# Kernel tuning notes

Hardware: AMD Instinct MI355X
Metric: run time of the kernel (lower is better)

## Reference

```python
import jax, jax.numpy as jnp
import numpy as np

B_, L_, D_MODEL = 2, 2048, 1024
D_INNER, D_STATE, DT_RANK, D_CONV = 2048, 16, 64, 4


def setup_inputs() -> dict:
    key = jax.random.key(0)
    ks = jax.random.split(key, 8)
    x = jax.random.normal(ks[0], (B_, L_, D_MODEL), dtype=jnp.float32)
    W_in = jax.random.normal(ks[1], (D_MODEL, 2 * D_INNER), dtype=jnp.float32) / np.sqrt(D_MODEL)
    conv_w = jax.random.normal(ks[2], (D_INNER, 1, D_CONV), dtype=jnp.float32) / np.sqrt(D_CONV)
    conv_b = jnp.zeros((D_INNER,), dtype=jnp.float32)
    W_x = jax.random.normal(ks[3], (D_INNER, DT_RANK + 2 * D_STATE), dtype=jnp.float32) / np.sqrt(D_INNER)
    W_dt = jax.random.normal(ks[4], (DT_RANK, D_INNER), dtype=jnp.float32) / np.sqrt(DT_RANK)
    b_dt = jax.random.normal(ks[5], (D_INNER,), dtype=jnp.float32) * 0.01
    A_log = jnp.log(jnp.broadcast_to(jnp.arange(1, D_STATE + 1, dtype=jnp.float32), (D_INNER, D_STATE)))
    D = jnp.ones((D_INNER,), dtype=jnp.float32)
    W_out = jax.random.normal(ks[6], (D_INNER, D_MODEL), dtype=jnp.float32) / np.sqrt(D_INNER)
    return {"x": x, "W_in": W_in, "conv_w": conv_w, "conv_b": conv_b, "W_x": W_x,
            "W_dt": W_dt, "b_dt": b_dt, "A_log": A_log, "D": D, "W_out": W_out}


def _mamba_fwd(x, W_in, conv_w, conv_b, W_x, W_dt, b_dt, A_log, D, W_out):
    b, l, d = x.shape
    x_and_res = x @ W_in                      # [b, l, 2*d_inner]
    xi, res = jnp.split(x_and_res, 2, axis=-1)
    # causal depthwise conv1d (torch pads d_conv-1 both sides then truncates -> left pad only)
    xc = jax.lax.conv_general_dilated(
        xi.transpose(0, 2, 1), conv_w, window_strides=(1,),
        padding=[(D_CONV - 1, 0)], feature_group_count=D_INNER,
        dimension_numbers=("NCH", "OIH", "NCH"))
    xc = (xc + conv_b[None, :, None]).transpose(0, 2, 1)  # [b, l, d_inner]
    xc = jax.nn.silu(xc)
    # SSM params
    x_dbl = xc @ W_x                           # [b, l, dt_rank + 2n]
    delta, Bm, Cm = jnp.split(x_dbl, [DT_RANK, DT_RANK + D_STATE], axis=-1)
    delta = jax.nn.softplus(delta @ W_dt + b_dt)          # [b, l, d_inner]
    A = -jnp.exp(A_log.astype(jnp.float32))               # [d_inner, n]
    deltaA = jnp.exp(jnp.einsum('bld,dn->bldn', delta, A))
    deltaB_u = jnp.einsum('bld,bln,bld->bldn', delta, Bm, xc)
    # sequential selective scan over l via lax.scan
    def step(h, inp):
        dA, dBu, c = inp           # [b,d,n], [b,d,n], [b,n]
        h = dA * h + dBu
        y = jnp.einsum('bdn,bn->bd', h, c)
        return h, y
    h0 = jnp.zeros((b, D_INNER, D_STATE), dtype=jnp.float32)
    _, ys = jax.lax.scan(step, h0, (deltaA.transpose(1, 0, 2, 3),
                                    deltaB_u.transpose(1, 0, 2, 3),
                                    Cm.transpose(1, 0, 2)))
    y = ys.transpose(1, 0, 2)                 # [b, l, d_inner]
    y = y + xc * D
    y = y * jax.nn.silu(res)
    return y @ W_out


def reference(x, W_in, conv_w, conv_b, W_x, W_dt, b_dt, A_log, D, W_out):
    return _mamba_fwd(x, W_in, conv_w, conv_b, W_x, W_dt, b_dt, A_log, D, W_out)
```

## Files before the change

### kernel.cpp

```cpp
#include <hip/hip_runtime.h>
#include <hip/hip_bf16.h>
#include <cstdint>


#define B_    2
#define L_    2048
#define DMODEL 1024
#define DINNER 2048
#define DSTATE 16
#define DTRANK 64
#define NC    16
#define CL    128

typedef short bf16x8 __attribute__((ext_vector_type(8)));
typedef float f32x4  __attribute__((ext_vector_type(4)));

__device__ __forceinline__ float sigmoidf_(float x) {
  return 1.f / (1.f + __expf(-x));
}
__device__ __forceinline__ float softplusf_(float x) {
  return fmaxf(x, 0.f) + log1pf(__expf(-fabsf(x)));
}
__device__ __forceinline__ unsigned short f2bf_rne(float x) {
  union { float f; unsigned int u; } v; v.f = x;
  unsigned int r = v.u + 0x7FFFu + ((v.u >> 16) & 1u);
  return (unsigned short)(r >> 16);
}
__device__ __forceinline__ float bf2f(unsigned short h) {
  union { float f; unsigned int u; } v; v.u = ((unsigned int)h) << 16;
  return v.f;
}
__device__ __forceinline__ void split3_a(float x, unsigned short* o) {
  unsigned short hi = f2bf_rne(x);
  unsigned short lo = f2bf_rne(x - bf2f(hi));
  o[0] = hi; o[1] = lo; o[2] = hi;
}
__device__ __forceinline__ void split3_b(float x, unsigned short* o) {
  unsigned short hi = f2bf_rne(x);
  unsigned short lo = f2bf_rne(x - bf2f(hi));
  o[0] = hi; o[1] = hi; o[2] = lo;
}

__device__ __forceinline__ void gload16(const void* g, void* l) {
  __builtin_amdgcn_global_load_lds(
      (const __attribute__((address_space(1))) void*)g,
      (__attribute__((address_space(3))) void*)l, 16, 0, 0);
}

template<int SPLITCOL>
__launch_bounds__(256)
__global__ void gemm_mfma_bf16(const unsigned short* __restrict__ A3,
                               const unsigned short* __restrict__ B3t,
                               float* __restrict__ outA,
                               float* __restrict__ outB,
                               int N, int K3)
{
  __shared__ unsigned short As[128 * 64];
  __shared__ unsigned short Bs[128 * 64];

  const int tid  = threadIdx.x;
  const int lane = tid & 63;
  const int wid  = tid >> 6;
  const int wr   = wid >> 1;
  const int wc   = wid & 1;
  const int m0   = blockIdx.y * 128;
  const int n0   = blockIdx.x * 128;

  const int srow = lane >> 3;
  const int scol = ((lane & 7) ^ srow) * 8;

  const unsigned short* gA = A3 + (size_t)(m0 + wid * 8 + srow) * K3 + scol;
  const unsigned short* gB = B3t + (size_t)(n0 + wid * 8 + srow) * K3 + scol;
  const size_t rs32 = (size_t)32 * K3;

  unsigned short* lA = &As[wid * 8 * 64];
  unsigned short* lB = &Bs[wid * 8 * 64];

  f32x4 acc[4][4];
#pragma unroll
  for (int i = 0; i < 4; ++i)
#pragma unroll
    for (int j = 0; j < 4; ++j) acc[i][j] = (f32x4){0.f, 0.f, 0.f, 0.f};

  const int KT = K3 >> 6;
  for (int kt = 0; kt < KT; ++kt) {
    const int k0 = kt << 6;
#pragma unroll
    for (int i = 0; i < 4; ++i) {
      gload16(gA + i * rs32 + k0, lA + i * 32 * 64);
      gload16(gB + i * rs32 + k0, lB + i * 32 * 64);
    }
    __syncthreads();

#pragma unroll
    for (int kk = 0; kk < 2; ++kk) {
      const int c16 = kk * 4 + (lane >> 4);
      bf16x8 a[4], b[4];
#pragma unroll
      for (int rb = 0; rb < 4; ++rb) {
        const int row = wr * 64 + rb * 16 + (lane & 15);
        a[rb] = *(const bf16x8*)&As[row * 64 + ((c16 ^ (row & 7)) << 3)];
        const int col = wc * 64 + rb * 16 + (lane & 15);
        b[rb] = *(const bf16x8*)&Bs[col * 64 + ((c16 ^ (col & 7)) << 3)];
      }
#pragma unroll
      for (int rb = 0; rb < 4; ++rb)
#pragma unroll
        for (int nb = 0; nb < 4; ++nb)
          acc[rb][nb] = __builtin_amdgcn_mfma_f32_16x16x32_bf16(
              a[rb], b[nb], acc[rb][nb], 0, 0, 0);
    }
    __syncthreads();
  }

  const int crow0 = (lane >> 4) * 4;
  const int ccol  = lane & 15;
#pragma unroll
  for (int rb = 0; rb < 4; ++rb) {
#pragma unroll
    for (int nb = 0; nb < 4; ++nb) {
      const int gc = n0 + wc * 64 + nb * 16 + ccol;
#pragma unroll
      for (int j = 0; j < 4; ++j) {
        const int gr = m0 + wr * 64 + rb * 16 + crow0 + j;
        const float v = acc[rb][nb][j];
        if (SPLITCOL > 0) {
          if (gc < SPLITCOL) outA[(size_t)gr * SPLITCOL + gc] = v;
          else               outB[(size_t)gr * SPLITCOL + (gc - SPLITCOL)] = v;
        } else {
          outA[(size_t)gr * N + gc] = v;
        }
      }
    }
  }
}

__launch_bounds__(256)
__global__ void split_a3(const float* __restrict__ in,
                         unsigned short* __restrict__ out)
{
  const int idx = blockIdx.x * 256 + threadIdx.x;
  const int row = idx >> 8;
  const int q   = idx & 255;
  float4 v = *(const float4*)&in[(size_t)row * DMODEL + q * 4];
  unsigned short buf[12] __attribute__((aligned(8)));
  split3_a(v.x, &buf[0]);
  split3_a(v.y, &buf[3]);
  split3_a(v.z, &buf[6]);
  split3_a(v.w, &buf[9]);
  unsigned short* o = out + (size_t)row * 3072 + q * 12;
#pragma unroll
  for (int j = 0; j < 3; ++j)
    *(ushort4*)&o[j * 4] = *(const ushort4*)&buf[j * 4];
}

__launch_bounds__(256)
__global__ void split_bt3(const float* __restrict__ B,
                          unsigned short* __restrict__ out,
                          int K, int N)
{
  __shared__ float T[64][65];
  const int n0 = blockIdx.x * 64;
  const int k0 = blockIdx.y * 64;
  const int t  = threadIdx.x;

  const int nl4 = (t & 15) * 4;
  const int klr = t >> 4;
#pragma unroll
  for (int i = 0; i < 4; ++i) {
    float4 v = *(const float4*)&B[(size_t)(k0 + klr + i * 16) * N + n0 + nl4];
    T[klr + i * 16][nl4 + 0] = v.x;
    T[klr + i * 16][nl4 + 1] = v.y;
    T[klr + i * 16][nl4 + 2] = v.z;
    T[klr + i * 16][nl4 + 3] = v.w;
  }
  __syncthreads();

  const int nl = t >> 2;
  const int kc = (t & 3) * 16;
  unsigned short buf[48] __attribute__((aligned(8)));
#pragma unroll
  for (int kk = 0; kk < 16; ++kk) split3_b(T[kc + kk][nl], &buf[kk * 3]);
  unsigned short* o = out + (size_t)(n0 + nl) * (3 * K) + 3 * (k0 + kc);
#pragma unroll
  for (int j = 0; j < 12; ++j)
    *(ushort4*)&o[j * 4] = *(const ushort4*)&buf[j * 4];
}

#define KS_   4
#define KCH   (DINNER / KS_)
__launch_bounds__(384)
__global__ void gemm_wx_splitk(const float* __restrict__ xc,
                               const float* __restrict__ wx,
                               float* __restrict__ part)
{
  const int ks = blockIdx.x;
  const int m0 = blockIdx.y * 16;
  const int t  = threadIdx.x;
  const int r  = t / 24;
  const int c  = (t % 24) * 4;
  const int k0 = ks * KCH;

  const float* arow = xc + (size_t)(m0 + r) * DINNER + k0;
  const float* wp   = wx + (size_t)k0 * 96 + c;

  float ax = 0.f, ay = 0.f, az = 0.f, aw = 0.f;
  for (int k = 0; k < KCH; k += 4) {
    float4 a  = *(const float4*)&arow[k];
    float4 w0 = *(const float4*)&wp[(size_t)(k + 0) * 96];
    float4 w1 = *(const float4*)&wp[(size_t)(k + 1) * 96];
    float4 w2 = *(const float4*)&wp[(size_t)(k + 2) * 96];
    float4 w3 = *(const float4*)&wp[(size_t)(k + 3) * 96];
    ax = fmaf(a.x, w0.x, ax); ax = fmaf(a.y, w1.x, ax);
    ax = fmaf(a.z, w2.x, ax); ax = fmaf(a.w, w3.x, ax);
    ay = fmaf(a.x, w0.y, ay); ay = fmaf(a.y, w1.y, ay);
    ay = fmaf(a.z, w2.y, ay); ay = fmaf(a.w, w3.y, ay);
    az = fmaf(a.x, w0.z, az); az = fmaf(a.y, w1.z, az);
    az = fmaf(a.z, w2.z, az); az = fmaf(a.w, w3.z, az);
    aw = fmaf(a.x, w0.w, aw); aw = fmaf(a.y, w1.w, aw);
    aw = fmaf(a.z, w2.w, aw); aw = fmaf(a.w, w3.w, aw);
  }
  float4 o = {ax, ay, az, aw};
  *(float4*)&part[((size_t)ks * 4096 + m0 + r) * 96 + c] = o;
}

__launch_bounds__(256)
__global__ void reduce_wx(const float* __restrict__ part,
                          float* __restrict__ xdbl)
{
  const int i = blockIdx.x * 256 + threadIdx.x;
  const size_t S = (size_t)4096 * 96 / 4;
  const float4* p = (const float4*)part;
  float4 a = p[i];
  float4 b = p[i + S];
  float4 c = p[i + 2 * S];
  float4 d = p[i + 3 * S];
  float4 o;
  o.x = (a.x + b.x) + (c.x + d.x);
  o.y = (a.y + b.y) + (c.y + d.y);
  o.z = (a.z + b.z) + (c.z + d.z);
  o.w = (a.w + b.w) + (c.w + d.w);
  ((float4*)xdbl)[i] = o;
}

template<int BM, int BN, int BK, int RG, int CG, int EPI>
__launch_bounds__(256)
__global__ void gemm_f32(const float* __restrict__ A, int lda,
                         const float* __restrict__ B, int ldb,
                         float* __restrict__ C, int ldc,
                         int M, int N, int K,
                         const float* __restrict__ bias)
{
  __shared__ float As[BK][BM + 4];
  __shared__ float Bs[BK][BN + 4];

  const int tid = threadIdx.x;
  const int tx = tid & 15;
  const int ty = tid >> 4;
  const int m0 = blockIdx.y * BM;
  const int n0 = blockIdx.x * BN;

  float acc[RG * 4][CG * 4];
#pragma unroll
  for (int i = 0; i < RG * 4; ++i)
#pragma unroll
    for (int j = 0; j < CG * 4; ++j) acc[i][j] = 0.f;

  const int KF4 = BK / 4;
  const int NF4 = BN / 4;

  for (int k0 = 0; k0 < K; k0 += BK) {
#pragma unroll
    for (int j = tid; j < BM * KF4; j += 256) {
      int row = j / KF4, kq = j % KF4;
      float4 v = *(const float4*)&A[(size_t)(m0 + row) * lda + k0 + kq * 4];
      As[kq * 4 + 0][row] = v.x;
      As[kq * 4 + 1][row] = v.y;
      As[kq * 4 + 2][row] = v.z;
      As[kq * 4 + 3][row] = v.w;
    }
#pragma unroll
    for (int j = tid; j < BK * NF4; j += 256) {
      int row = j / NF4, nq = j % NF4;
      int c = n0 + nq * 4;
      float4 v;
      if (c + 3 < N) {
        v = *(const float4*)&B[(size_t)(k0 + row) * ldb + c];
      } else {
        const float* bp = &B[(size_t)(k0 + row) * ldb];
        v.x = (c + 0 < N) ? bp[c + 0] : 0.f;
        v.y = (c + 1 < N) ? bp[c + 1] : 0.f;
        v.z = (c + 2 < N) ? bp[c + 2] : 0.f;
        v.w = (c + 3 < N) ? bp[c + 3] : 0.f;
      }
      *(float4*)&Bs[row][nq * 4] = v;
    }
    __syncthreads();

#pragma unroll
    for (int k = 0; k < BK; ++k) {
      float a[RG][4], b[CG][4];
#pragma unroll
      for (int g = 0; g < RG; ++g) {
        float4 va = *(const float4*)&As[k][g * (BM / RG) + ty * 4];
        a[g][0] = va.x; a[g][1] = va.y; a[g][2] = va.z; a[g][3] = va.w;
      }
#pragma unroll
      for (int h = 0; h < CG; ++h) {
        float4 vb = *(const float4*)&Bs[k][h * (BN / CG) + tx * 4];
        b[h][0] = vb.x; b[h][1] = vb.y; b[h][2] = vb.z; b[h][3] = vb.w;
      }
#pragma unroll
      for (int g = 0; g < RG; ++g)
#pragma unroll
        for (int i = 0; i < 4; ++i)
#pragma unroll
          for (int h = 0; h < CG; ++h)
#pragma unroll
            for (int j = 0; j < 4; ++j)
              acc[g * 4 + i][h * 4 + j] =
                  fmaf(a[g][i], b[h][j], acc[g * 4 + i][h * 4 + j]);
    }
    __syncthreads();
  }

#pragma unroll
  for (int g = 0; g < RG; ++g) {
#pragma unroll
    for (int i = 0; i < 4; ++i) {
      int r = m0 + g * (BM / RG) + ty * 4 + i;
#pragma unroll
      for (int h = 0; h < CG; ++h) {
        int c = n0 + h * (BN / CG) + tx * 4;
        float4 v;
        v.x = acc[g * 4 + i][h * 4 + 0];
        v.y = acc[g * 4 + i][h * 4 + 1];
        v.z = acc[g * 4 + i][h * 4 + 2];
        v.w = acc[g * 4 + i][h * 4 + 3];
        if (c + 3 < N) {
          if (EPI == 1) {
            v.x = softplusf_(v.x + bias[c + 0]);
            v.y = softplusf_(v.y + bias[c + 1]);
            v.z = softplusf_(v.z + bias[c + 2]);
            v.w = softplusf_(v.w + bias[c + 3]);
          }
          *(float4*)&C[(size_t)r * ldc + c] = v;
        } else {
          float vv[4] = {v.x, v.y, v.z, v.w};
#pragma unroll
          for (int j = 0; j < 4; ++j)
            if (c + j < N) {
              float o = vv[j];
              if (EPI == 1) o = softplusf_(o + bias[c + j]);
              C[(size_t)r * ldc + c + j] = o;
            }
        }
      }
    }
  }
}

__launch_bounds__(256)
__global__ void conv_silu(const float* __restrict__ xi,
                          const float* __restrict__ conv_w,
                          const float* __restrict__ conv_b,
                          float* __restrict__ xc)
{
  const int total = B_ * L_ * (DINNER / 4);
  for (int idx = blockIdx.x * blockDim.x + threadIdx.x; idx < total;
       idx += gridDim.x * blockDim.x) {
    int d4 = idx & (DINNER / 4 - 1);
    int l = (idx >> 9) & (L_ - 1);
    int b = idx >> 20;
    int d = d4 * 4;

    float w[4][4];
#pragma unroll
    for (int c = 0; c < 4; ++c) {
      float4 wv = *(const float4*)&conv_w[(d + c) * 4];
      w[c][0] = wv.x; w[c][1] = wv.y; w[c][2] = wv.z; w[c][3] = wv.w;
    }
    float4 bv = *(const float4*)&conv_b[d];
    float s[4] = {bv.x, bv.y, bv.z, bv.w};
#pragma unroll
    for (int t = 0; t < 4; ++t) {
      int ls = l - 3 + t;
      if (ls >= 0) {
        float4 xv = *(const float4*)&xi[(size_t)(b * L_ + ls) * DINNER + d];
        s[0] = fmaf(w[0][t], xv.x, s[0]);
        s[1] = fmaf(w[1][t], xv.y, s[1]);
        s[2] = fmaf(w[2][t], xv.z, s[2]);
        s[3] = fmaf(w[3][t], xv.w, s[3]);
      }
    }
    float4 o;
    o.x = s[0] * sigmoidf_(s[0]);
    o.y = s[1] * sigmoidf_(s[1]);
    o.z = s[2] * sigmoidf_(s[2]);
    o.w = s[3] * sigmoidf_(s[3]);
    *(float4*)&xc[(size_t)idx * 4] = o;
  }
}

__launch_bounds__(256)
__global__ void scan_pass1(const float* __restrict__ delta,
                           const float* __restrict__ xc,
                           const float* __restrict__ xdbl,
                           const float* __restrict__ A_log,
                           float* __restrict__ Pbuf,
                           float* __restrict__ Qbuf)
{
  const int blk = blockIdx.x;
  const int b = blk >> 7;
  const int c = (blk >> 3) & (NC - 1);
  const int d = ((blk & 7) << 8) + threadIdx.x;

  float An[DSTATE];
#pragma unroll
  for (int n = 0; n < DSTATE; ++n) An[n] = -__expf(A_log[d * DSTATE + n]);

  __shared__ float bs[CL][DSTATE];
  const size_t bL = (size_t)b * L_;
  const int l0 = c * CL;
  for (int j = threadIdx.x; j < CL * 4; j += 256) {
    int step = j >> 2, q = j & 3;
    *(float4*)&bs[step][q * 4] =
        *(const float4*)&xdbl[(bL + l0 + step) * 96 + DTRANK + q * 4];
  }
  __syncthreads();

  float P[DSTATE], q[DSTATE];
#pragma unroll
  for (int n = 0; n < DSTATE; ++n) { P[n] = 1.f; q[n] = 0.f; }

  for (int i = 0; i < CL; ++i) {
    const size_t bl = bL + l0 + i;
    float dv = delta[bl * DINNER + d];
    float dx = dv * xc[bl * DINNER + d];
#pragma unroll
    for (int n = 0; n < DSTATE; ++n) {
      float dA = __expf(dv * An[n]);
      P[n] *= dA;
      q[n] = fmaf(dA, q[n], dx * bs[i][n]);
    }
  }
  const size_t base = (((size_t)b * NC + c) * DSTATE) * DINNER + d;
#pragma unroll
  for (int n = 0; n < DSTATE; ++n) {
    Pbuf[base + (size_t)n * DINNER] = P[n];
    Qbuf[base + (size_t)n * DINNER] = q[n];
  }
}

__launch_bounds__(256)
__global__ void scan_combine(const float* __restrict__ Pbuf,
                             const float* __restrict__ Qbuf,
                             float* __restrict__ Hini)
{
  const int idx = blockIdx.x * 256 + threadIdx.x;
  const int d = idx & (DINNER - 1);
  const int n = (idx >> 11) & (DSTATE - 1);
  const int b = idx >> 15;

  float h = 0.f;
#pragma unroll
  for (int c = 0; c < NC; ++c) {
    const size_t off = (((size_t)b * NC + c) * DSTATE + n) * DINNER + d;
    Hini[off] = h;
    h = fmaf(Pbuf[off], h, Qbuf[off]);
  }
}

__launch_bounds__(256)
__global__ void scan_pass2(const float* __restrict__ delta,
                           const float* __restrict__ xc,
                           const float* __restrict__ res,
                           const float* __restrict__ xdbl,
                           const float* __restrict__ A_log,
                           const float* __restrict__ Dvec,
                           const float* __restrict__ Hini,
                           unsigned short* __restrict__ yg3)
{
  const int blk = blockIdx.x;
  const int b = blk >> 7;
  const int c = (blk >> 3) & (NC - 1);
  const int d = ((blk & 7) << 8) + threadIdx.x;

  float An[DSTATE];
#pragma unroll
  for (int n = 0; n < DSTATE; ++n) An[n] = -__expf(A_log[d * DSTATE + n]);
  const float Dd = Dvec[d];

  float h[DSTATE];
  const size_t base = (((size_t)b * NC + c) * DSTATE) * DINNER + d;
#pragma unroll
  for (int n = 0; n < DSTATE; ++n) h[n] = Hini[base + (size_t)n * DINNER];

  __shared__ float bc[CL][2 * DSTATE];
  const size_t bL = (size_t)b * L_;
  const int l0 = c * CL;
  for (int j = threadIdx.x; j < CL * 8; j += 256) {
    int step = j >> 3, q = j & 7;
    *(float4*)&bc[step][q * 4] =
        *(const float4*)&xdbl[(bL + l0 + step) * 96 + DTRANK + q * 4];
  }
  __syncthreads();

  for (int i = 0; i < CL; ++i) {
    const size_t bl = bL + l0 + i;
    float dv = delta[bl * DINNER + d];
    float xv = xc[bl * DINNER + d];
    float rv = res[bl * DINNER + d];
    float dx = dv * xv;
    float y = 0.f;
#pragma unroll
    for (int n = 0; n < DSTATE; ++n) {
      float dA = __expf(dv * An[n]);
      h[n] = fmaf(dA, h[n], dx * bc[i][n]);
      y = fmaf(h[n], bc[i][DSTATE + n], y);
    }
    float v = (y + xv * Dd) * (rv * sigmoidf_(rv));
    unsigned short hi = f2bf_rne(v);
    unsigned short lo = f2bf_rne(v - bf2f(hi));
    const size_t o = bl * 6144 + 3 * (size_t)d;
    yg3[o + 0] = hi; yg3[o + 1] = lo; yg3[o + 2] = hi;
  }
}

extern "C" void kernel_launch(void* const* d_in, const int* in_sizes, int n_in,
                              void* d_out, int out_size, void* d_ws,
                              size_t ws_size, hipStream_t stream)
{
  const float* x      = (const float*)d_in[0];
  const float* W_in   = (const float*)d_in[1];
  const float* conv_w = (const float*)d_in[2];
  const float* conv_b = (const float*)d_in[3];
  const float* W_x    = (const float*)d_in[4];
  const float* W_dt   = (const float*)d_in[5];
  const float* b_dt   = (const float*)d_in[6];
  const float* A_log  = (const float*)d_in[7];
  const float* Dv     = (const float*)d_in[8];
  const float* W_out  = (const float*)d_in[9];
  float* out = (float*)d_out;

  float* ws = (float*)d_ws;
  float* xi    = ws;
  float* res   = ws + 8388608;
  float* xc    = ws + 16777216;
  float* xdbl  = ws + 25165824;
  float* Pbuf  = ws + 25559040;
  float* Qbuf  = ws + 26607616;
  float* Hini  = ws + 27656192;
  unsigned short* yg3      = (unsigned short*)(ws + 28704768);
  unsigned short* bt3_wout = (unsigned short*)(ws + 41287680);
  unsigned short* a3_x     = (unsigned short*)(ws + 16777216);
  unsigned short* bt3_win  = (unsigned short*)(ws + 23068672);
  float* delta = ws;
  float* part  = ws;

  const int M = B_ * L_;

  split_a3<<<4096, 256, 0, stream>>>(x, a3_x);
  split_bt3<<<dim3(4096 / 64, 1024 / 64), 256, 0, stream>>>(W_in, bt3_win,
                                                            1024, 4096);

  gemm_mfma_bf16<2048><<<dim3(32, 32), 256, 0, stream>>>(
      a3_x, bt3_win, xi, res, 4096, 3072);

  split_bt3<<<dim3(1024 / 64, 2048 / 64), 256, 0, stream>>>(W_out, bt3_wout,
                                                            2048, 1024);

  conv_silu<<<4096, 256, 0, stream>>>(xi, conv_w, conv_b, xc);

  gemm_wx_splitk<<<dim3(KS_, M / 16), 384, 0, stream>>>(xc, W_x, part);
  reduce_wx<<<384, 256, 0, stream>>>(part, xdbl);

  gemm_f32<128, 128, 16, 2, 2, 1>
      <<<dim3(DINNER / 128, M / 128), 256, 0, stream>>>(
          xdbl, 96, W_dt, DINNER, delta, DINNER, M, DINNER, DTRANK, b_dt);

  scan_pass1<<<B_ * NC * (DINNER / 256), 256, 0, stream>>>(
      delta, xc, xdbl, A_log, Pbuf, Qbuf);
  scan_combine<<<(B_ * DSTATE * DINNER) / 256, 256, 0, stream>>>(
      Pbuf, Qbuf, Hini);
  scan_pass2<<<B_ * NC * (DINNER / 256), 256, 0, stream>>>(
      delta, xc, res, xdbl, A_log, Dv, Hini, yg3);

  gemm_mfma_bf16<0><<<dim3(8, 32), 256, 0, stream>>>(
      yg3, bt3_wout, out, nullptr, 1024, 6144);
}
```

Baseline: 703.5 us.

## Double scan chunk count, narrow out-proj GEMM tile, add workgroup swizzle

```diff
diff --git a/kernel.cpp b/kernel.cpp
--- a/kernel.cpp
+++ b/kernel.cpp
@@ -9,8 +9,8 @@
 #define DINNER 2048
 #define DSTATE 16
 #define DTRANK 64
-#define NC    16
-#define CL    128
+#define NC    32
+#define CL    64
 
 typedef short bf16x8 __attribute__((ext_vector_type(8)));
 typedef float f32x4  __attribute__((ext_vector_type(4)));
@@ -47,7 +47,7 @@
       (__attribute__((address_space(3))) void*)l, 16, 0, 0);
 }
 
-template<int SPLITCOL>
+template<int BN, int SPLITCOL>
 __launch_bounds__(256)
 __global__ void gemm_mfma_bf16(const unsigned short* __restrict__ A3,
                                const unsigned short* __restrict__ B3t,
@@ -55,16 +55,22 @@
                                float* __restrict__ outB,
                                int N, int K3)
 {
+  constexpr int NR = BN / 32;
   __shared__ unsigned short As[128 * 64];
-  __shared__ unsigned short Bs[128 * 64];
+  __shared__ unsigned short Bs[BN * 64];
 
   const int tid  = threadIdx.x;
   const int lane = tid & 63;
   const int wid  = tid >> 6;
   const int wr   = wid >> 1;
   const int wc   = wid & 1;
-  const int m0   = blockIdx.y * 128;
-  const int n0   = blockIdx.x * 128;
+
+  const int NX   = gridDim.x;
+  const int nwg  = NX * gridDim.y;
+  const int flat = blockIdx.y * NX + blockIdx.x;
+  const int swz  = (flat & 7) * (nwg >> 3) + (flat >> 3);
+  const int m0   = (swz / NX) * 128;
+  const int n0   = (swz % NX) * BN;
 
   const int srow = lane >> 3;
   const int scol = ((lane & 7) ^ srow) * 8;
@@ -76,37 +82,41 @@
   unsigned short* lA = &As[wid * 8 * 64];
   unsigned short* lB = &Bs[wid * 8 * 64];
 
-  f32x4 acc[4][4];
+  f32x4 acc[4][NR];
 #pragma unroll
   for (int i = 0; i < 4; ++i)
 #pragma unroll
-    for (int j = 0; j < 4; ++j) acc[i][j] = (f32x4){0.f, 0.f, 0.f, 0.f};
+    for (int j = 0; j < NR; ++j) acc[i][j] = (f32x4){0.f, 0.f, 0.f, 0.f};
 
   const int KT = K3 >> 6;
   for (int kt = 0; kt < KT; ++kt) {
     const int k0 = kt << 6;
 #pragma unroll
-    for (int i = 0; i < 4; ++i) {
+    for (int i = 0; i < 4; ++i)
       gload16(gA + i * rs32 + k0, lA + i * 32 * 64);
+#pragma unroll
+    for (int i = 0; i < BN / 32; ++i)
       gload16(gB + i * rs32 + k0, lB + i * 32 * 64);
-    }
     __syncthreads();
 
 #pragma unroll
     for (int kk = 0; kk < 2; ++kk) {
       const int c16 = kk * 4 + (lane >> 4);
-      bf16x8 a[4], b[4];
+      bf16x8 a[4], b[NR];
 #pragma unroll
       for (int rb = 0; rb < 4; ++rb) {
         const int row = wr * 64 + rb * 16 + (lane & 15);
         a[rb] = *(const bf16x8*)&As[row * 64 + ((c16 ^ (row & 7)) << 3)];
-        const int col = wc * 64 + rb * 16 + (lane & 15);
-        b[rb] = *(const bf16x8*)&Bs[col * 64 + ((c16 ^ (col & 7)) << 3)];
+      }
+#pragma unroll
+      for (int nb = 0; nb < NR; ++nb) {
+        const int col = wc * (BN / 2) + nb * 16 + (lane & 15);
+        b[nb] = *(const bf16x8*)&Bs[col * 64 + ((c16 ^ (col & 7)) << 3)];
       }
 #pragma unroll
       for (int rb = 0; rb < 4; ++rb)
 #pragma unroll
-        for (int nb = 0; nb < 4; ++nb)
+        for (int nb = 0; nb < NR; ++nb)
           acc[rb][nb] = __builtin_amdgcn_mfma_f32_16x16x32_bf16(
               a[rb], b[nb], acc[rb][nb], 0, 0, 0);
     }
@@ -118,8 +128,8 @@
 #pragma unroll
   for (int rb = 0; rb < 4; ++rb) {
 #pragma unroll
-    for (int nb = 0; nb < 4; ++nb) {
-      const int gc = n0 + wc * 64 + nb * 16 + ccol;
+    for (int nb = 0; nb < NR; ++nb) {
+      const int gc = n0 + wc * (BN / 2) + nb * 16 + ccol;
 #pragma unroll
       for (int j = 0; j < 4; ++j) {
         const int gr = m0 + wr * 64 + rb * 16 + crow0 + j;
@@ -411,7 +421,7 @@
                            float* __restrict__ Qbuf)
 {
   const int blk = blockIdx.x;
-  const int b = blk >> 7;
+  const int b = blk >> 8;
   const int c = (blk >> 3) & (NC - 1);
   const int d = ((blk & 7) << 8) + threadIdx.x;
 
@@ -482,7 +492,7 @@
                            unsigned short* __restrict__ yg3)
 {
   const int blk = blockIdx.x;
-  const int b = blk >> 7;
+  const int b = blk >> 8;
   const int c = (blk >> 3) & (NC - 1);
   const int d = ((blk & 7) << 8) + threadIdx.x;
 
@@ -548,10 +558,10 @@
   float* res   = ws + 8388608;
   float* xc    = ws + 16777216;
   float* xdbl  = ws + 25165824;
-  float* Pbuf  = ws + 25559040;
-  float* Qbuf  = ws + 26607616;
-  float* Hini  = ws + 27656192;
+  float* Hini  = ws + 25559040;
   unsigned short* yg3      = (unsigned short*)(ws + 28704768);
+  float* Pbuf  = ws + 28704768;
+  float* Qbuf  = ws + 30801920;
   unsigned short* bt3_wout = (unsigned short*)(ws + 41287680);
   unsigned short* a3_x     = (unsigned short*)(ws + 16777216);
   unsigned short* bt3_win  = (unsigned short*)(ws + 23068672);
@@ -564,7 +574,7 @@
   split_bt3<<<dim3(4096 / 64, 1024 / 64), 256, 0, stream>>>(W_in, bt3_win,
                                                             1024, 4096);
 
-  gemm_mfma_bf16<2048><<<dim3(32, 32), 256, 0, stream>>>(
+  gemm_mfma_bf16<128, 2048><<<dim3(32, 32), 256, 0, stream>>>(
       a3_x, bt3_win, xi, res, 4096, 3072);
 
   split_bt3<<<dim3(1024 / 64, 2048 / 64), 256, 0, stream>>>(W_out, bt3_wout,
@@ -586,6 +596,6 @@
   scan_pass2<<<B_ * NC * (DINNER / 256), 256, 0, stream>>>(
       delta, xc, res, xdbl, A_log, Dv, Hini, yg3);
 
-  gemm_mfma_bf16<0><<<dim3(8, 32), 256, 0, stream>>>(
+  gemm_mfma_bf16<64, 0><<<dim3(16, 32), 256, 0, stream>>>(
       yg3, bt3_wout, out, nullptr, 1024, 6144);
 }
```

Result: faster. 615.4 us (-12.5%).
